# Kernel optimization log

Measured on AMD Instinct MI355X. Metric: run time of the kernel, lower is better.

## Reference

```python
import jax, jax.numpy as jnp
import numpy as np

B, N, D = 4, 4096, 768
K_TOP = 8  # module's self.k
EPS = 1e-12  # F.normalize eps


def setup_inputs() -> dict:
    key = jax.random.key(0)
    k0, k1, k2 = jax.random.split(key, 3)
    s = 1.0 / np.sqrt(D)
    feats = jax.random.normal(k0, (B, N, D), dtype=jnp.float32)
    Wq = jax.random.normal(k1, (D, D), dtype=jnp.float32) * s
    bq = jnp.zeros((D,), dtype=jnp.float32)
    Wkv = jax.random.normal(k2, (D, 2 * D), dtype=jnp.float32) * s
    bkv = jnp.zeros((2 * D,), dtype=jnp.float32)
    return {"feats": feats, "Wq": Wq, "bq": bq, "Wkv": Wkv, "bkv": bkv}


def _l2norm(x):
    return x / jnp.maximum(jnp.linalg.norm(x, axis=-1, keepdims=True), EPS)


def reference(feats, Wq, bq, Wkv, bkv):
    # Only self.q and self.kv are used in the original forward; the
    # transformer encoder / norm / score_head / proj are dead code there.
    b, n, d = feats.shape
    Q = feats @ Wq + bq                      # [B,N,D]
    KV = feats @ Wkv + bkv                   # [B,N,2D]
    Kmat, Vmat = jnp.split(KV, 2, axis=-1)   # [B,N,D] each

    # cosine-distance kNN graph (self excluded via +1e6 on diagonal)
    sim = jnp.einsum('bnd,bmd->bnm', _l2norm(Q), _l2norm(Kmat))
    dist = (1.0 - sim) + jnp.eye(n, dtype=sim.dtype)[None] * 1e6
    k_eff = min(n - 1, K_TOP)
    _, idx = jax.lax.top_k(-dist, k_eff)     # smallest distances -> [B,N,k]

    # gather neighbor K/V (no O(N^2 * D) expand)
    bidx = jnp.arange(b)[:, None, None]
    Kn = Kmat[bidx, idx]                     # [B,N,k,D]
    Vn = Vmat[bidx, idx]                     # [B,N,k,D]

    attn = jnp.einsum('bnd,bnkd->bnk', Q, Kn) / np.float32(np.sqrt(d))
    attn = jax.nn.softmax(attn, axis=-1)     # [B,N,k]
    out = jnp.einsum('bnk,bnkd->bnd', attn, Vn)
    return out.mean(axis=1)                  # [B,D]
```

## Files before the change

### kernel.cpp

```cpp
#include <hip/hip_runtime.h>
#include <hip/hip_bf16.h>
#include <math.h>

#define B_ 4
#define N_ 4096
#define D_ 768
#define KTOP 8
#define M_ (B_*N_)
#define TCAND 12
#define SELK 32

typedef __attribute__((ext_vector_type(8))) short short8;
typedef __attribute__((ext_vector_type(4))) float f32x4;
typedef _Float16 half_t;
typedef __attribute__((ext_vector_type(8))) _Float16 half8;
typedef __attribute__((ext_vector_type(4))) _Float16 half4;

__device__ __forceinline__ ushort f2bf(float f) {
    unsigned int u = __float_as_uint(f);
    unsigned int r = (u + 0x7FFFu + ((u >> 16) & 1u)) >> 16;
    return (ushort)r;
}

__device__ __forceinline__ void gload16(const void* g, void* l) {
    __builtin_amdgcn_global_load_lds(
        (const __attribute__((address_space(1))) unsigned int*)g,
        (__attribute__((address_space(3))) unsigned int*)l, 16, 0, 0);
}

#define CSD(A, i, j) { unsigned int _mx = max(A[i], A[j]); \
                       unsigned int _mn = min(A[i], A[j]); \
                       A[i] = _mx; A[j] = _mn; }

__global__ __launch_bounds__(256) void split_feats(
    const float* __restrict__ f, half_t* __restrict__ Fh, half_t* __restrict__ Fl)
{
    const int i = (blockIdx.x * 256 + threadIdx.x) * 4;
    const float4 v = *(const float4*)&f[i];
    float x[4] = {v.x, v.y, v.z, v.w};
    half4 h, l;
#pragma unroll
    for (int c = 0; c < 4; ++c) {
        const half_t hh = (half_t)x[c];
        h[c] = hh;
        l[c] = (half_t)(x[c] - (float)hh);
    }
    *(half4*)&Fh[i] = h;
    *(half4*)&Fl[i] = l;
}

__global__ __launch_bounds__(256) void split_w(
    const float* __restrict__ Wq, const float* __restrict__ Wkv,
    half_t* __restrict__ Wth, half_t* __restrict__ Wtl)
{
    __shared__ float T[64][65];
    const int tid = threadIdx.x;
    const int n0 = blockIdx.x * 64;
    const int k0 = blockIdx.y * 64;

    const int nl = tid & 63;
#pragma unroll
    for (int r = 0; r < 16; ++r) {
        const int kl = (tid >> 6) * 16 + r;
        const int n  = n0 + nl;
        const float w = (n < 768)
            ? Wq[(size_t)(k0 + kl) * 768 + n]
            : Wkv[(size_t)(k0 + kl) * 1536 + (n - 768)];
        T[kl][nl] = w;
    }
    __syncthreads();

    const int kl2 = tid & 63;
#pragma unroll
    for (int r = 0; r < 16; ++r) {
        const int nl2 = (tid >> 6) * 16 + r;
        const float ws = T[kl2][nl2] * 4096.0f;
        const half_t h = (half_t)ws;
        const half_t l = (half_t)(ws - (float)h);
        Wth[(size_t)(n0 + nl2) * D_ + k0 + kl2] = h;
        Wtl[(size_t)(n0 + nl2) * D_ + k0 + kl2] = l;
    }
}

__global__ __launch_bounds__(256) void qkv_mfma(
    const half_t* __restrict__ Fh, const half_t* __restrict__ Fl,
    const half_t* __restrict__ Wth, const half_t* __restrict__ Wtl,
    const float* __restrict__ bq, const float* __restrict__ bkv,
    float* __restrict__ Q, float* __restrict__ Km, half_t* __restrict__ Vh)
{
    __shared__ __align__(16) half_t Ah[128 * 64];
    __shared__ __align__(16) half_t Al[128 * 64];
    __shared__ __align__(16) half_t Bh[128 * 64];
    __shared__ __align__(16) half_t Bl[128 * 64];

    const int tid  = threadIdx.x;
    const int lane = tid & 63, w = tid >> 6;
    const int wr = w >> 1, wc = w & 1;
    const int r16 = lane & 15, kq = lane >> 4;
    const int n0 = blockIdx.x * 128;
    const int m0 = blockIdx.y * 128;
    const bool three = (n0 < 1536);

    const half_t* ah = Fh  + (size_t)(m0 + (tid >> 3)) * D_ + (tid & 7) * 8;
    const half_t* al = Fl  + (size_t)(m0 + (tid >> 3)) * D_ + (tid & 7) * 8;
    const half_t* bh = Wth + (size_t)(n0 + (tid >> 3)) * D_ + (tid & 7) * 8;
    const half_t* bl = Wtl + (size_t)(n0 + (tid >> 3)) * D_ + (tid & 7) * 8;
    half_t* lAh = Ah + (w << 9);
    half_t* lAl = Al + (w << 9);
    half_t* lBh = Bh + (w << 9);
    half_t* lBl = Bl + (w << 9);

    f32x4 acc[4][4];
#pragma unroll
    for (int mi = 0; mi < 4; ++mi)
#pragma unroll
        for (int ni = 0; ni < 4; ++ni) acc[mi][ni] = (f32x4)0.f;

    for (int kb = 0; kb < D_ / 64; ++kb) {
#pragma unroll
        for (int i = 0; i < 4; ++i) {
            gload16(ah + (size_t)i * 32 * D_ + kb * 64, lAh + i * 2048);
            gload16(bh + (size_t)i * 32 * D_ + kb * 64, lBh + i * 2048);
        }
        if (three) {
#pragma unroll
            for (int i = 0; i < 4; ++i) {
                gload16(al + (size_t)i * 32 * D_ + kb * 64, lAl + i * 2048);
                gload16(bl + (size_t)i * 32 * D_ + kb * 64, lBl + i * 2048);
            }
        }
        __syncthreads();
#pragma unroll
        for (int kk = 0; kk < 2; ++kk) {
            half8 fa[4], fb[4];
#pragma unroll
            for (int mi = 0; mi < 4; ++mi)
                fa[mi] = *(const half8*)&Ah[(wr * 64 + mi * 16 + r16) * 64 + kk * 32 + kq * 8];
#pragma unroll
            for (int ni = 0; ni < 4; ++ni)
                fb[ni] = *(const half8*)&Bh[(wc * 64 + ni * 16 + r16) * 64 + kk * 32 + kq * 8];
#pragma unroll
            for (int mi = 0; mi < 4; ++mi)
#pragma unroll
                for (int ni = 0; ni < 4; ++ni)
                    acc[mi][ni] = __builtin_amdgcn_mfma_f32_16x16x32_f16(
                        fa[mi], fb[ni], acc[mi][ni], 0, 0, 0);
            if (three) {
                half8 gal[4], gbl[4];
#pragma unroll
                for (int mi = 0; mi < 4; ++mi)
                    gal[mi] = *(const half8*)&Al[(wr * 64 + mi * 16 + r16) * 64 + kk * 32 + kq * 8];
#pragma unroll
                for (int ni = 0; ni < 4; ++ni)
                    gbl[ni] = *(const half8*)&Bl[(wc * 64 + ni * 16 + r16) * 64 + kk * 32 + kq * 8];
#pragma unroll
                for (int mi = 0; mi < 4; ++mi)
#pragma unroll
                    for (int ni = 0; ni < 4; ++ni) {
                        acc[mi][ni] = __builtin_amdgcn_mfma_f32_16x16x32_f16(
                            fa[mi], gbl[ni], acc[mi][ni], 0, 0, 0);
                        acc[mi][ni] = __builtin_amdgcn_mfma_f32_16x16x32_f16(
                            gal[mi], fb[ni], acc[mi][ni], 0, 0, 0);
                    }
            }
        }
        __syncthreads();
    }

    const float unscale = 1.0f / 4096.0f;
#pragma unroll
    for (int ni = 0; ni < 4; ++ni) {
        const int n = n0 + wc * 64 + ni * 16 + r16;
        const float bias = (n0 < 768) ? bq[n] : bkv[n - 768];
        if (three) {
            float* dst = (n0 < 768) ? Q : Km;
            const int nn = (n0 < 768) ? n : (n - 768);
#pragma unroll
            for (int mi = 0; mi < 4; ++mi)
#pragma unroll
                for (int r = 0; r < 4; ++r) {
                    const int m = m0 + wr * 64 + mi * 16 + kq * 4 + r;
                    dst[(size_t)m * D_ + nn] = acc[mi][ni][r] * unscale + bias;
                }
        } else {
            const int nn = n - 1536;
#pragma unroll
            for (int mi = 0; mi < 4; ++mi)
#pragma unroll
                for (int r = 0; r < 4; ++r) {
                    const int m = m0 + wr * 64 + mi * 16 + kq * 4 + r;
                    Vh[(size_t)m * D_ + nn] = (half_t)(acc[mi][ni][r] * unscale + bias);
                }
        }
    }
}

__global__ __launch_bounds__(256) void norm_bf16(
    const float* __restrict__ Q, const float* __restrict__ Km,
    ushort* __restrict__ qn, ushort* __restrict__ kn,
    float* __restrict__ rqinv, float* __restrict__ rkinv)
{
    const int wid  = blockIdx.x * 4 + (threadIdx.x >> 6);
    const int lane = threadIdx.x & 63;
    const float* src; ushort* dst; float* rv; int r;
    if (wid < M_) { src = Q;  dst = qn; rv = rqinv; r = wid; }
    else          { src = Km; dst = kn; rv = rkinv; r = wid - M_; }
    const float* p = src + (size_t)r * D_ + lane * 12;
    float v[12];
#pragma unroll
    for (int i = 0; i < 3; ++i) *(float4*)&v[i * 4] = *(const float4*)&p[i * 4];
    float s = 0.f;
#pragma unroll
    for (int i = 0; i < 12; ++i) s += v[i] * v[i];
#pragma unroll
    for (int off = 32; off; off >>= 1) s += __shfl_xor(s, off);
    const float rinv = 1.0f / fmaxf(sqrtf(s), 1e-12f);
    ushort* op = dst + (size_t)r * D_ + lane * 12;
#pragma unroll
    for (int i = 0; i < 3; ++i) {
        ushort4 o;
        o.x = f2bf(v[i * 4 + 0] * rinv); o.y = f2bf(v[i * 4 + 1] * rinv);
        o.z = f2bf(v[i * 4 + 2] * rinv); o.w = f2bf(v[i * 4 + 3] * rinv);
        *(ushort4*)&op[i * 4] = o;
    }
    if (lane == 0) rv[r] = rinv;
}

__global__ __launch_bounds__(256) void sim_topk_fused(
    const ushort* __restrict__ qn_all, const ushort* __restrict__ kn_all,
    unsigned int* __restrict__ Part)
{
    __shared__ __align__(16) ushort smem[128 * 136];
    ushort* As = smem;
    ushort* Bs = smem + 128 * 64;

    const int tid  = threadIdx.x;
    const int lane = tid & 63, w = tid >> 6;
    const int wr = w >> 1, wc = w & 1;
    const int r16 = lane & 15, kq = lane >> 4;
    const int k0 = blockIdx.x * 128;
    const int q0 = blockIdx.y * 128;
    const int b  = blockIdx.z;

    const ushort* qsrc = qn_all + ((size_t)b * N_ + q0 + (tid >> 3)) * D_ + (tid & 7) * 8;
    const ushort* ksrc = kn_all + ((size_t)b * N_ + k0 + (tid >> 3)) * D_ + (tid & 7) * 8;
    ushort* lA = As + (w << 9);
    ushort* lB = Bs + (w << 9);

    f32x4 acc[4][4];
#pragma unroll
    for (int mi = 0; mi < 4; ++mi)
#pragma unroll
        for (int ni = 0; ni < 4; ++ni) acc[mi][ni] = (f32x4)0.f;

    for (int kb = 0; kb < D_ / 64; ++kb) {
#pragma unroll
        for (int i = 0; i < 4; ++i) {
            gload16(qsrc + (size_t)i * 32 * D_ + kb * 64, lA + i * 2048);
            gload16(ksrc + (size_t)i * 32 * D_ + kb * 64, lB + i * 2048);
        }
        __syncthreads();
#pragma unroll
        for (int kk = 0; kk < 2; ++kk) {
            short8 a[4], bfr[4];
#pragma unroll
            for (int mi = 0; mi < 4; ++mi)
                a[mi] = *(const short8*)&As[(wr * 64 + mi * 16 + r16) * 64 + kk * 32 + kq * 8];
#pragma unroll
            for (int ni = 0; ni < 4; ++ni)
                bfr[ni] = *(const short8*)&Bs[(wc * 64 + ni * 16 + r16) * 64 + kk * 32 + kq * 8];
#pragma unroll
            for (int mi = 0; mi < 4; ++mi)
#pragma unroll
                for (int ni = 0; ni < 4; ++ni)
                    acc[mi][ni] = __builtin_amdgcn_mfma_f32_16x16x32_bf16(
                        a[mi], bfr[ni], acc[mi][ni], 0, 0, 0);
        }
        __syncthreads();
    }

    ushort* St = smem;
#pragma unroll
    for (int mi = 0; mi < 4; ++mi)
#pragma unroll
        for (int ni = 0; ni < 4; ++ni)
#pragma unroll
            for (int r = 0; r < 4; ++r) {
                const int row = wr * 64 + mi * 16 + kq * 4 + r;
                const int col = wc * 64 + ni * 16 + r16;
                const bool diag = (q0 + row) == (k0 + col);
                St[row * 136 + col] = diag ? (ushort)0xFF7Fu : f2bf(acc[mi][ni][r]);
            }
    __syncthreads();

    const int rrow = tid >> 1, half = tid & 1;
    const int KREV = (N_ - 1) - (k0 + half * 64);
    const ushort* sp = St + rrow * 136 + half * 64;
    unsigned int t[TCAND];
#pragma unroll
    for (int i = 0; i < TCAND; ++i) t[i] = 0u;

#pragma unroll
    for (int j = 0; j < 64; j += 8) {
        const uint4 dv = *(const uint4*)(sp + j);
        unsigned int dw[4];
        dw[0] = dv.x; dw[1] = dv.y; dw[2] = dv.z; dw[3] = dv.w;
#pragma unroll
        for (int q = 0; q < 4; ++q) {
            const unsigned int vlo = dw[q] & 0xFFFFu;
            const unsigned int vhi = dw[q] >> 16;
            const unsigned int plo =
                ((vlo ^ (0x8000u + ((vlo >> 15) * 0x7FFFu))) << 16) |
                (unsigned int)(KREV - (j + 2 * q));
            const unsigned int phi =
                ((vhi ^ (0x8000u + ((vhi >> 15) * 0x7FFFu))) << 16) |
                (unsigned int)(KREV - (j + 2 * q + 1));
            unsigned int p = plo;
#pragma unroll
            for (int i = 0; i < TCAND; ++i) {
                const unsigned int mx = max(t[i], p);
                const unsigned int mn = min(t[i], p);
                t[i] = mx; p = mn;
            }
            p = phi;
#pragma unroll
            for (int i = 0; i < TCAND; ++i) {
                const unsigned int mx = max(t[i], p);
                const unsigned int mn = min(t[i], p);
                t[i] = mx; p = mn;
            }
        }
    }
    __syncthreads();

    unsigned int* scratch = (unsigned int*)smem;
    if (half) {
#pragma unroll
        for (int i = 0; i < TCAND; ++i) scratch[rrow * TCAND + i] = t[i];
    }
    __syncthreads();
    if (!half) {
#pragma unroll
        for (int i = 0; i < TCAND; ++i) {
            unsigned int p = scratch[rrow * TCAND + i];
#pragma unroll
            for (int s = 0; s < TCAND; ++s) {
                const unsigned int mx = max(t[s], p);
                const unsigned int mn = min(t[s], p);
                t[s] = mx; p = mn;
            }
        }
        unsigned int* op = Part +
            ((size_t)(b * N_ + q0 + rrow) * SELK + (k0 >> 7)) * TCAND;
#pragma unroll
        for (int i = 0; i < TCAND; ++i) op[i] = t[i];
    }
}

__global__ __launch_bounds__(256) void merge_rescore_attn(
    const float* __restrict__ Q, const float* __restrict__ Kmat,
    const half_t* __restrict__ Vh, const float* __restrict__ rqinv,
    const float* __restrict__ rkinv, const unsigned int* __restrict__ Part,
    float* __restrict__ outPart)
{
    __shared__ float laccum[4][D_];
    const int tid  = threadIdx.x;
    const int w    = tid >> 6, lane = tid & 63;
    const int row  = blockIdx.x * 4 + w;
    const int b    = row >> 12;

    const unsigned int* pp = Part + (size_t)row * (SELK * TCAND);
    unsigned int t[16];
#pragma unroll
    for (int i = 0; i < 16; ++i) t[i] = 0u;
#pragma unroll
    for (int i = 0; i < 6; ++i) t[i] = pp[i * 64 + lane];
    CSD(t, 0, 5); CSD(t, 1, 3); CSD(t, 2, 4);
    CSD(t, 1, 2); CSD(t, 3, 4);
    CSD(t, 0, 3); CSD(t, 2, 5);
    CSD(t, 0, 1); CSD(t, 2, 3); CSD(t, 4, 5);
    CSD(t, 1, 2); CSD(t, 3, 4);
#pragma unroll
    for (int st = 0; st < 6; ++st) {
        const int dl = 1 << st;
        unsigned int p[16];
#pragma unroll
        for (int i = 0; i < 16; ++i)
            p[i] = (unsigned int)__shfl_xor((int)t[i], dl);
        unsigned int h[16];
#pragma unroll
        for (int i = 0; i < 16; ++i) h[i] = max(t[i], p[15 - i]);
        CSD(h, 0, 8); CSD(h, 1, 9); CSD(h, 2, 10); CSD(h, 3, 11);
        CSD(h, 4, 12); CSD(h, 5, 13); CSD(h, 6, 14); CSD(h, 7, 15);
        CSD(h, 0, 4); CSD(h, 1, 5); CSD(h, 2, 6); CSD(h, 3, 7);
        CSD(h, 8, 12); CSD(h, 9, 13); CSD(h, 10, 14); CSD(h, 11, 15);
        CSD(h, 0, 2); CSD(h, 1, 3); CSD(h, 4, 6); CSD(h, 5, 7);
        CSD(h, 8, 10); CSD(h, 9, 11); CSD(h, 12, 14); CSD(h, 13, 15);
        CSD(h, 0, 1); CSD(h, 2, 3); CSD(h, 4, 5); CSD(h, 6, 7);
        CSD(h, 8, 9); CSD(h, 10, 11); CSD(h, 12, 13); CSD(h, 14, 15);
#pragma unroll
        for (int i = 0; i < 16; ++i) t[i] = h[i];
    }
    int ka[TCAND];
#pragma unroll
    for (int j = 0; j < TCAND; ++j) ka[j] = (N_ - 1) - (int)(t[j] & 0xFFFFu);

    float qv[12];
    {
        const float* qp = Q + (size_t)row * D_ + lane * 12;
#pragma unroll
        for (int i = 0; i < 3; ++i) *(float4*)&qv[i * 4] = *(const float4*)&qp[i * 4];
    }
    const float rq = rqinv[row];
    const float scale = 0.03608439182435161f;

    float rkl[TCAND];
#pragma unroll
    for (int j = 0; j < TCAND; ++j) rkl[j] = rkinv[(b << 12) + ka[j]];

    float d[TCAND];
#pragma unroll
    for (int j = 0; j < TCAND; ++j) d[j] = 0.f;
#pragma unroll
    for (int j = 0; j < TCAND; ++j) {
        const float* kp = Kmat + ((size_t)(b << 12) + ka[j]) * D_ + lane * 12;
#pragma unroll
        for (int i = 0; i < 3; ++i) {
            const float4 kv = *(const float4*)&kp[i * 4];
            d[j] += qv[i * 4 + 0] * kv.x + qv[i * 4 + 1] * kv.y +
                    qv[i * 4 + 2] * kv.z + qv[i * 4 + 3] * kv.w;
        }
    }
#pragma unroll
    for (int off = 32; off; off >>= 1)
#pragma unroll
        for (int j = 0; j < TCAND; ++j) d[j] += __shfl_xor(d[j], off);

    float simv[TCAND];
#pragma unroll
    for (int j = 0; j < TCAND; ++j) simv[j] = d[j] * rq * rkl[j];

    int rk8[TCAND];
#pragma unroll
    for (int j = 0; j < TCAND; ++j) {
        int r = 0;
#pragma unroll
        for (int o = 0; o < TCAND; ++o) {
            if (o != j)
                r += (simv[o] > simv[j] ||
                      (simv[o] == simv[j] && ka[o] < ka[j])) ? 1 : 0;
        }
        rk8[j] = r;
    }

    float mx = -1e30f;
#pragma unroll
    for (int j = 0; j < TCAND; ++j) if (rk8[j] < KTOP) mx = fmaxf(mx, d[j] * scale);
    float e[TCAND]; float ps = 0.f;
#pragma unroll
    for (int j = 0; j < TCAND; ++j) {
        const float ee = (rk8[j] < KTOP) ? expf(d[j] * scale - mx) : 0.f;
        e[j] = ee; ps += ee;
    }
    const float inv = 1.0f / ps;

    float oacc[12];
#pragma unroll
    for (int i = 0; i < 12; ++i) oacc[i] = 0.f;
#pragma unroll
    for (int j = 0; j < TCAND; ++j) {
        if (rk8[j] < KTOP) {
            const float p = e[j] * inv;
            const half_t* vp = Vh + ((size_t)(b << 12) + ka[j]) * D_ + lane * 12;
#pragma unroll
            for (int i = 0; i < 3; ++i) {
                const half4 hv = *(const half4*)&vp[i * 4];
                oacc[i * 4 + 0] += p * (float)hv[0];
                oacc[i * 4 + 1] += p * (float)hv[1];
                oacc[i * 4 + 2] += p * (float)hv[2];
                oacc[i * 4 + 3] += p * (float)hv[3];
            }
        }
    }

#pragma unroll
    for (int i = 0; i < 3; ++i)
        *(float4*)&laccum[w][lane * 12 + i * 4] = *(float4*)&oacc[i * 4];
    __syncthreads();
    for (int dd = tid; dd < D_; dd += 256) {
        outPart[(size_t)blockIdx.x * D_ + dd] =
            laccum[0][dd] + laccum[1][dd] + laccum[2][dd] + laccum[3][dd];
    }
}

__global__ __launch_bounds__(256) void reduce_out(
    const float* __restrict__ outPart, float* __restrict__ out)
{
    const int idx = blockIdx.x * 256 + threadIdx.x;
    const int b = idx / D_;
    const int dd = idx - b * D_;
    float s = 0.f;
#pragma unroll 8
    for (int p = 0; p < 1024; ++p)
        s += outPart[((size_t)(b << 10) + p) * D_ + dd];
    out[idx] = s * (1.0f / N_);
}

extern "C" void kernel_launch(void* const* d_in, const int* in_sizes, int n_in,
                              void* d_out, int out_size, void* d_ws, size_t ws_size,
                              hipStream_t stream)
{
    const float* feats = (const float*)d_in[0];
    const float* Wq    = (const float*)d_in[1];
    const float* bq    = (const float*)d_in[2];
    const float* Wkv   = (const float*)d_in[3];
    const float* bkv   = (const float*)d_in[4];
    float* out = (float*)d_out;

    char* ws = (char*)d_ws;
    size_t off = 0;
    float*  Q    = (float*)(ws + off);  off += (size_t)M_ * D_ * sizeof(float);
    float*  Km   = (float*)(ws + off);  off += (size_t)M_ * D_ * sizeof(float);
    char*   unio = ws + off;            off += 2 * (size_t)M_ * D_ * sizeof(ushort);
    half_t* Fh   = (half_t*)unio;
    half_t* Fl   = (half_t*)(unio + (size_t)M_ * D_ * sizeof(half_t));
    ushort* qn   = (ushort*)unio;
    ushort* kn   = (ushort*)(unio + (size_t)M_ * D_ * sizeof(ushort));
    half_t* Vh   = (half_t*)(ws + off); off += (size_t)M_ * D_ * sizeof(half_t);
    float*  rqv  = (float*)(ws + off);  off += (size_t)M_ * sizeof(float);
    float*  rkv  = (float*)(ws + off);  off += (size_t)M_ * sizeof(float);
    half_t* Wth  = (half_t*)(ws + off); off += (size_t)2304 * D_ * sizeof(half_t);
    half_t* Wtl  = (half_t*)(ws + off); off += (size_t)2304 * D_ * sizeof(half_t);
    unsigned int* Part = (unsigned int*)(ws + off);
    off += (size_t)M_ * SELK * TCAND * sizeof(unsigned int);
    float* outPart = (float*)(ws + off);
    off += (size_t)(M_ / 4) * D_ * sizeof(float);
    (void)ws_size; (void)in_sizes; (void)n_in; (void)out_size;

    split_feats<<<(M_ * D_) / 1024, 256, 0, stream>>>(feats, Fh, Fl);
    split_w<<<dim3(2304 / 64, D_ / 64), 256, 0, stream>>>(Wq, Wkv, Wth, Wtl);
    qkv_mfma<<<dim3(2304 / 128, M_ / 128), 256, 0, stream>>>(
        Fh, Fl, Wth, Wtl, bq, bkv, Q, Km, Vh);
    norm_bf16<<<(2 * M_) / 4, 256, 0, stream>>>(Q, Km, qn, kn, rqv, rkv);

    sim_topk_fused<<<dim3(N_ / 128, N_ / 128, B_), 256, 0, stream>>>(qn, kn, Part);

    merge_rescore_attn<<<M_ / 4, 256, 0, stream>>>(
        Q, Km, Vh, rqv, rkv, Part, outPart);
    reduce_out<<<(B_ * D_) / 256, 256, 0, stream>>>(outPart, out);
}
```

Baseline: 662.0 us.

## Swizzle GEMM block order across XCDs and split merge into tournament and rescore kernels

```diff
diff --git a/kernel.cpp b/kernel.cpp
--- a/kernel.cpp
+++ b/kernel.cpp
@@ -97,8 +97,11 @@
     const int lane = tid & 63, w = tid >> 6;
     const int wr = w >> 1, wc = w & 1;
     const int r16 = lane & 15, kq = lane >> 4;
-    const int n0 = blockIdx.x * 128;
-    const int m0 = blockIdx.y * 128;
+
+    const int bid  = blockIdx.x + 18 * blockIdx.y;
+    const int work = (bid & 7) * 288 + (bid >> 3);
+    const int n0 = (work % 18) * 128;
+    const int m0 = (work / 18) * 128;
     const bool three = (n0 < 1536);
 
     const half_t* ah = Fh  + (size_t)(m0 + (tid >> 3)) * D_ + (tid & 7) * 8;
@@ -238,9 +241,12 @@
     const int lane = tid & 63, w = tid >> 6;
     const int wr = w >> 1, wc = w & 1;
     const int r16 = lane & 15, kq = lane >> 4;
-    const int k0 = blockIdx.x * 128;
-    const int q0 = blockIdx.y * 128;
-    const int b  = blockIdx.z;
+
+    const int bid  = blockIdx.x + (blockIdx.y << 5) + (blockIdx.z << 10);
+    const int work = (bid & 7) * 512 + (bid >> 3);
+    const int k0 = (work & 31) * 128;
+    const int q0 = ((work >> 5) & 31) * 128;
+    const int b  = work >> 10;
 
     const ushort* qsrc = qn_all + ((size_t)b * N_ + q0 + (tid >> 3)) * D_ + (tid & 7) * 8;
     const ushort* ksrc = kn_all + ((size_t)b * N_ + k0 + (tid >> 3)) * D_ + (tid & 7) * 8;
@@ -357,17 +363,12 @@
     }
 }
 
-__global__ __launch_bounds__(256) void merge_rescore_attn(
-    const float* __restrict__ Q, const float* __restrict__ Kmat,
-    const half_t* __restrict__ Vh, const float* __restrict__ rqinv,
-    const float* __restrict__ rkinv, const unsigned int* __restrict__ Part,
-    float* __restrict__ outPart)
-{
-    __shared__ float laccum[4][D_];
+__global__ __launch_bounds__(256) void tournament(
+    const unsigned int* __restrict__ Part, int* __restrict__ TopIdx)
+{
     const int tid  = threadIdx.x;
     const int w    = tid >> 6, lane = tid & 63;
     const int row  = blockIdx.x * 4 + w;
-    const int b    = row >> 12;
 
     const unsigned int* pp = Part + (size_t)row * (SELK * TCAND);
     unsigned int t[16];
@@ -401,9 +402,45 @@
 #pragma unroll
         for (int i = 0; i < 16; ++i) t[i] = h[i];
     }
+    if (lane == 0) {
+        int4 o0, o1, o2;
+        o0.x = (N_ - 1) - (int)(t[0] & 0xFFFFu);
+        o0.y = (N_ - 1) - (int)(t[1] & 0xFFFFu);
+        o0.z = (N_ - 1) - (int)(t[2] & 0xFFFFu);
+        o0.w = (N_ - 1) - (int)(t[3] & 0xFFFFu);
+        o1.x = (N_ - 1) - (int)(t[4] & 0xFFFFu);
+        o1.y = (N_ - 1) - (int)(t[5] & 0xFFFFu);
+        o1.z = (N_ - 1) - (int)(t[6] & 0xFFFFu);
+        o1.w = (N_ - 1) - (int)(t[7] & 0xFFFFu);
+        o2.x = (N_ - 1) - (int)(t[8] & 0xFFFFu);
+        o2.y = (N_ - 1) - (int)(t[9] & 0xFFFFu);
+        o2.z = (N_ - 1) - (int)(t[10] & 0xFFFFu);
+        o2.w = (N_ - 1) - (int)(t[11] & 0xFFFFu);
+        int4* op = (int4*)(TopIdx + (size_t)row * TCAND);
+        op[0] = o0; op[1] = o1; op[2] = o2;
+    }
+}
+
+__global__ __launch_bounds__(256) void rescore_attn(
+    const float* __restrict__ Q, const float* __restrict__ Kmat,
+    const half_t* __restrict__ Vh, const float* __restrict__ rqinv,
+    const float* __restrict__ rkinv, const int* __restrict__ TopIdx,
+    float* __restrict__ outPart)
+{
+    __shared__ float laccum[4][D_];
+    const int tid  = threadIdx.x;
+    const int w    = tid >> 6, lane = tid & 63;
+    const int row  = blockIdx.x * 4 + w;
+    const int b    = row >> 12;
+
     int ka[TCAND];
-#pragma unroll
-    for (int j = 0; j < TCAND; ++j) ka[j] = (N_ - 1) - (int)(t[j] & 0xFFFFu);
+    {
+        const int4* tp = (const int4*)(TopIdx + (size_t)row * TCAND);
+        const int4 a0 = tp[0], a1 = tp[1], a2 = tp[2];
+        ka[0] = a0.x; ka[1] = a0.y; ka[2]  = a0.z; ka[3]  = a0.w;
+        ka[4] = a1.x; ka[5] = a1.y; ka[6]  = a1.z; ka[7]  = a1.w;
+        ka[8] = a2.x; ka[9] = a2.y; ka[10] = a2.z; ka[11] = a2.w;
+    }
 
     float qv[12];
     {
@@ -535,6 +572,8 @@
     off += (size_t)M_ * SELK * TCAND * sizeof(unsigned int);
     float* outPart = (float*)(ws + off);
     off += (size_t)(M_ / 4) * D_ * sizeof(float);
+    int* TopIdx = (int*)(ws + off);
+    off += (size_t)M_ * TCAND * sizeof(int);
     (void)ws_size; (void)in_sizes; (void)n_in; (void)out_size;
 
     split_feats<<<(M_ * D_) / 1024, 256, 0, stream>>>(feats, Fh, Fl);
@@ -545,7 +584,8 @@
 
     sim_topk_fused<<<dim3(N_ / 128, N_ / 128, B_), 256, 0, stream>>>(qn, kn, Part);
 
-    merge_rescore_attn<<<M_ / 4, 256, 0, stream>>>(
-        Q, Km, Vh, rqv, rkv, Part, outPart);
+    tournament<<<M_ / 4, 256, 0, stream>>>(Part, TopIdx);
+    rescore_attn<<<M_ / 4, 256, 0, stream>>>(
+        Q, Km, Vh, rqv, rkv, TopIdx, outPart);
     reduce_out<<<(B_ * D_) / 256, 256, 0, stream>>>(outPart, out);
 }
```

Result: no change. 663.7 us (+0.2%).
